# Kernel tuning notes

Hardware: AMD Instinct MI355X
Metric: run time of the kernel (lower is better)

Reference implementation:

```python
import jax, jax.numpy as jnp
import numpy as np

K = 3  # deform kernel size; stride = K//2 = 1, pad = K%2 = 1


def _conv3x3(x, w, b):
    y = jax.lax.conv_general_dilated(x, w, (1, 1), [(1, 1), (1, 1)],
                                     dimension_numbers=('NCHW', 'OIHW', 'NCHW'))
    return y + b[None, :, None, None]


def _channel_attention(x, w1, b1, w2, b2):
    # RCAN channel attention: GAP -> 1x1 conv -> ReLU -> 1x1 conv -> sigmoid -> scale
    y = jnp.mean(x, axis=(2, 3))                 # [N, C]
    y = jax.nn.relu(y @ w1.T + b1)               # [N, C//16]
    y = jax.nn.sigmoid(y @ w2.T + b2)            # [N, C]
    return x * y[:, :, None, None]


def _bilinear_gather(x, py, px):
    # x: [N,C,H,W]; py/px: [N,Ho,Wo] float sampling coords; zero padding outside.
    H, W = x.shape[2], x.shape[3]
    y0 = jnp.floor(py); x0 = jnp.floor(px)
    wy1 = py - y0; wx1 = px - x0
    wy0 = 1.0 - wy1; wx0 = 1.0 - wx1

    def corner(yi, xi):
        valid = (yi >= 0) & (yi <= H - 1) & (xi >= 0) & (xi <= W - 1)
        yc = jnp.clip(yi, 0, H - 1).astype(jnp.int32)
        xc = jnp.clip(xi, 0, W - 1).astype(jnp.int32)
        g = jax.vmap(lambda xb, yb, xb2: xb[:, yb, xb2])(x, yc, xc)  # [N,C,Ho,Wo]
        return g * valid[:, None, :, :].astype(x.dtype)

    return (corner(y0, x0) * (wy0 * wx0)[:, None]
            + corner(y0, x0 + 1.0) * (wy0 * wx1)[:, None]
            + corner(y0 + 1.0, x0) * (wy1 * wx0)[:, None]
            + corner(y0 + 1.0, x0 + 1.0) * (wy1 * wx1)[:, None])


def _deform_conv(x, offset, w, b, k=K, stride=1, pad=1):
    # torchvision deform_conv2d, offset_groups=1, no modulation mask.
    N, C, H, W = x.shape
    Ho = (H + 2 * pad - k) // stride + 1
    Wo = (W + 2 * pad - k) // stride + 1
    base_y = (jnp.arange(Ho) * stride - pad).astype(x.dtype)
    base_x = (jnp.arange(Wo) * stride - pad).astype(x.dtype)
    acc = jnp.zeros((N, w.shape[0], Ho, Wo), x.dtype)
    for i in range(k):
        for j in range(k):
            idx = i * k + j
            # torchvision layout: channel 2*idx is dy, 2*idx+1 is dx
            py = base_y[None, :, None] + i + offset[:, 2 * idx]
            px = base_x[None, None, :] + j + offset[:, 2 * idx + 1]
            sampled = _bilinear_gather(x, py, px)          # [N,C,Ho,Wo]
            acc = acc + jnp.einsum('nchw,oc->nohw', sampled, w[:, :, i, j])
    return acc + b[None, :, None, None]


def setup_inputs() -> dict:
    key = jax.random.key(0)
    ks = jax.random.split(key, 24)
    N, Cin, H, W = 8, 64, 192, 192
    Cout, sq = 64, Cin // 16
    s = 0.05
    inp = {
        'x': jax.random.normal(ks[0], (N, Cin, H, W), jnp.float32),
        'ref_x': jax.random.normal(ks[1], (N, 3, H, W), jnp.float32),
        'ref_w': jax.random.normal(ks[2], (Cin, 12, 3, 3), jnp.float32) * s,
        'ref_b': jnp.zeros((Cin,), jnp.float32),
        'off_w1': jax.random.normal(ks[3], (Cin, 2 * Cin, 3, 3), jnp.float32) * s,
        'off_b1': jnp.zeros((Cin,), jnp.float32),
        'ca1_w1': jax.random.normal(ks[4], (sq, Cin), jnp.float32) * s,
        'ca1_b1': jnp.zeros((sq,), jnp.float32),
        'ca1_w2': jax.random.normal(ks[5], (Cin, sq), jnp.float32) * s,
        'ca1_b2': jnp.zeros((Cin,), jnp.float32),
        'off_w2': jax.random.normal(ks[6], (Cin, Cin, 3, 3), jnp.float32) * s,
        'off_b2': jnp.zeros((Cin,), jnp.float32),
        'ca2_w1': jax.random.normal(ks[7], (sq, Cin), jnp.float32) * s,
        'ca2_b1': jnp.zeros((sq,), jnp.float32),
        'ca2_w2': jax.random.normal(ks[8], (Cin, sq), jnp.float32) * s,
        'ca2_b2': jnp.zeros((Cin,), jnp.float32),
        'off_w3': jax.random.normal(ks[9], (2 * K * K, Cin, 3, 3), jnp.float32) * 0.01,
        'off_b3': jnp.zeros((2 * K * K,), jnp.float32),
        'dcn_w': jax.random.normal(ks[10], (Cout, Cin, K, K), jnp.float32) * s,
        'dcn_b': jnp.zeros((Cout,), jnp.float32),
        'rgb_w': jax.random.normal(ks[11], (3, Cout, 3, 3), jnp.float32) * s,
        'rgb_b': jnp.zeros((3,), jnp.float32),
    }
    return inp


def reference(x, ref_x, ref_w, ref_b, off_w1, off_b1, ca1_w1, ca1_b1, ca1_w2, ca1_b2,
              off_w2, off_b2, ca2_w1, ca2_b1, ca2_w2, ca2_b2, off_w3, off_b3,
              dcn_w, dcn_b, rgb_w, rgb_b):
    # ref branch: 4-fold flip augmentation concat -> conv -> relu
    ref_cat = jnp.concatenate([ref_x, jnp.flip(ref_x, 2), jnp.flip(ref_x, 3),
                               jnp.flip(ref_x, (2, 3))], axis=1)
    ref_f = jax.nn.relu(_conv3x3(ref_cat, ref_w, ref_b))
    # offset branch
    t = jnp.concatenate([x, ref_f], axis=1)
    t = jax.nn.relu(_conv3x3(t, off_w1, off_b1))
    t = _channel_attention(t, ca1_w1, ca1_b1, ca1_w2, ca1_b2)
    t = jax.nn.relu(_conv3x3(t, off_w2, off_b2))
    t = _channel_attention(t, ca2_w1, ca2_b1, ca2_w2, ca2_b2)
    offset = _conv3x3(t, off_w3, off_b3)        # [N, 2*K*K, H, W]
    mask = offset
    xo = jax.nn.relu(_deform_conv(x, offset, dcn_w, dcn_b))
    rgb = _conv3x3(xo, rgb_w, rgb_b)
    return (xo, rgb, mask, offset)
```

## Files before the change

kernel.cpp:

```cpp
#include <hip/hip_runtime.h>
#include <hip/hip_bf16.h>
#include <math.h>

#define HH 192
#define WW 192
#define HW (192*192)

typedef __attribute__((ext_vector_type(8))) short bfrag;
typedef __attribute__((ext_vector_type(4))) float ffrag;

__device__ __forceinline__ float bf2f(ushort u){
    union { unsigned int i; float f; } c; c.i = ((unsigned int)u) << 16; return c.f;
}
__device__ __forceinline__ ushort f2bf(float f){
    __hip_bfloat16 h = __float2bfloat16(f);
    return *reinterpret_cast<ushort*>(&h);
}

__global__ __launch_bounds__(256)
void k_prep(const float* __restrict__ x, const float* __restrict__ rx,
            ushort* __restrict__ xbf, ushort* __restrict__ rcbf){
    const int n = blockIdx.y;
    const int tid = threadIdx.x;
    if (blockIdx.z == 0){
        __shared__ ushort sT[256*64];
        const int px0 = blockIdx.x * 256;
        for (int c = 0; c < 64; ++c){
            float v = x[((size_t)(n*64 + c))*HW + px0 + tid];
            int slot = (((c >> 3) ^ (tid & 7)) << 3) + (c & 7);
            sT[tid*64 + slot] = f2bf(v);
        }
        __syncthreads();
        for (int r = 0; r < 8; ++r){
            int u = r*256 + tid;
            int pl = u >> 3, g = u & 7;
            uint4 v = *(const uint4*)&sT[pl*64 + ((g ^ (pl & 7)) << 3)];
            *(uint4*)(xbf + ((size_t)n*HW + px0 + pl)*64 + g*8) = v;
        }
    } else {
        const int px = blockIdx.x*256 + tid;
        const int y = px / WW, xx = px - y*WW;
        ushort v[32];
#pragma unroll
        for (int m = 0; m < 4; ++m){
            int ry = (m & 1) ? (HH-1-y) : y;
            int rxp = (m & 2) ? (WW-1-xx) : xx;
#pragma unroll
            for (int c = 0; c < 3; ++c)
                v[m*3+c] = f2bf(rx[((size_t)(n*3+c))*HW + ry*WW + rxp]);
        }
#pragma unroll
        for (int j = 12; j < 32; ++j) v[j] = 0;
#pragma unroll
        for (int k = 0; k < 4; ++k)
            *(uint4*)(rcbf + ((size_t)n*HW + px)*32 + k*8) = *(uint4*)&v[k*8];
    }
}

__global__ void k_wfrag_all(const float* __restrict__ w0, const float* __restrict__ w1,
                            const float* __restrict__ w2, const float* __restrict__ w3,
                            const float* __restrict__ w4, const float* __restrict__ w5,
                            ushort* __restrict__ f0, ushort* __restrict__ f1,
                            ushort* __restrict__ f2, ushort* __restrict__ f3,
                            ushort* __restrict__ f4, ushort* __restrict__ f5){
    const float* w; ushort* wf; int cin_real, ncb, cout_real, mt;
    switch (blockIdx.y){
        case 0: w=w0; wf=f0; cin_real=12;  ncb=1; cout_real=64; mt=4; break;
        case 1: w=w1; wf=f1; cin_real=128; ncb=4; cout_real=64; mt=4; break;
        case 2: w=w2; wf=f2; cin_real=64;  ncb=2; cout_real=64; mt=4; break;
        case 3: w=w3; wf=f3; cin_real=64;  ncb=2; cout_real=18; mt=2; break;
        case 4: w=w4; wf=f4; cin_real=64;  ncb=2; cout_real=64; mt=4; break;
        default:w=w5; wf=f5; cin_real=64;  ncb=2; cout_real=3;  mt=1; break;
    }
    int idx = blockIdx.x*256 + threadIdx.x;
    int total = ncb*9*mt*512;
    if (idx >= total) return;
    int e = idx & 7;
    int lane = (idx >> 3) & 63;
    int rest = idx >> 9;
    int mtl = rest % mt;
    int tap = (rest / mt) % 9;
    int cb  = rest / (mt*9);
    int cout = mtl*16 + (lane & 15);
    int cin  = cb*32 + ((lane >> 4) << 3) + e;
    float v = 0.f;
    if (cout < cout_real && cin < cin_real)
        v = w[((size_t)cout*cin_real + cin)*9 + tap];
    wf[idx] = f2bf(v);
}

template<int NCB, int MT, bool SCALE, bool CONCAT, bool RELU, int OM, bool GAPP>
__device__ __forceinline__
void conv_body(const ushort* __restrict__ in0, const ushort* __restrict__ in1,
               const ushort* __restrict__ wf, const float* __restrict__ bias,
               const float* __restrict__ scale,
               ushort* __restrict__ obf, float* __restrict__ of0, float* __restrict__ of1,
               float* __restrict__ part, int cout_real)
{
    __shared__ ushort sXt[18*18*32];
    __shared__ float sG[4][4][16];
    __shared__ ushort sOut[(OM & 1) ? 8*16*64 : 1];
    const int tid = threadIdx.x;
    const int lane = tid & 63;
    const int wv = tid >> 6;
    const int n = blockIdx.z;
    const int ty0 = blockIdx.y*16, tx0 = blockIdx.x*16;
    const int lx = lane & 15;
    const int lg = lane >> 4;

    ffrag acc[MT][4];
#pragma unroll
    for (int mt = 0; mt < MT; ++mt)
#pragma unroll
        for (int q = 0; q < 4; ++q) acc[mt][q] = (ffrag){0.f,0.f,0.f,0.f};

    for (int cb = 0; cb < NCB; ++cb){
        __syncthreads();
        for (int u = tid; u < 1296; u += 256){
            int yy = u / 72; int rr = u - yy*72; int xx = rr >> 2; int g = rr & 3;
            int gy = ty0 - 1 + yy, gx = tx0 - 1 + xx;
            uint4 val = make_uint4(0,0,0,0);
            if (gy >= 0 && gy < HH && gx >= 0 && gx < WW){
                const ushort* src; int ch; int stride;
                if constexpr (CONCAT){
                    src = (cb < 2) ? in0 : in1;
                    ch = (cb & 1)*32 + g*8;
                    stride = 64;
                } else {
                    src = in0; ch = cb*32 + g*8; stride = NCB*32;
                }
                val = *(const uint4*)(src + ((size_t)n*HW + gy*WW + gx)*stride + ch);
                if constexpr (SCALE){
                    ushort* e = (ushort*)&val;
                    int cb8 = cb*32 + g*8;
#pragma unroll
                    for (int j = 0; j < 8; ++j)
                        e[j] = f2bf(bf2f(e[j]) * scale[n*64 + cb8 + j]);
                }
            }
            *(uint4*)&sXt[((yy*18 + xx)*4 + (g ^ ((xx >> 1) & 3)))*8] = val;
        }
        __syncthreads();

        const bfrag* wbase = (const bfrag*)wf + (size_t)cb*9*MT*64 + lane;
        bfrag a[MT];
#pragma unroll
        for (int mt = 0; mt < MT; ++mt) a[mt] = wbase[mt*64];

#pragma unroll
        for (int tap = 0; tap < 9; ++tap){
            const int ky = tap / 3, kx = tap % 3;
            bfrag an[MT];
            if (tap < 8){
#pragma unroll
                for (int mt = 0; mt < MT; ++mt) an[mt] = wbase[(tap+1)*MT*64 + mt*64];
            }
#pragma unroll
            for (int q = 0; q < 4; ++q){
                const int yl = wv*4 + q + ky;
                const int xl = lx + kx;
                bfrag b = *(const bfrag*)&sXt[((yl*18 + xl)*4 + (lg ^ ((xl >> 1) & 3)))*8];
#pragma unroll
                for (int mt = 0; mt < MT; ++mt)
                    acc[mt][q] = __builtin_amdgcn_mfma_f32_16x16x32_bf16(a[mt], b, acc[mt][q], 0, 0, 0);
            }
            if (tap < 8){
#pragma unroll
                for (int mt = 0; mt < MT; ++mt) a[mt] = an[mt];
            }
        }
    }
    const int gx = tx0 + lx;
    float psum[MT][4];
    if constexpr (GAPP){
#pragma unroll
        for (int mt = 0; mt < MT; ++mt)
#pragma unroll
            for (int j = 0; j < 4; ++j) psum[mt][j] = 0.f;
    }

    if constexpr (OM & 1){
#pragma unroll
        for (int pass = 0; pass < 2; ++pass){
            if ((wv >> 1) == pass){
#pragma unroll
                for (int mt = 0; mt < MT; ++mt){
                    const int co0 = mt*16 + lg*4;
                    const int t = mt*2 + (lg >> 1);
                    const int h = lg & 1;
#pragma unroll
                    for (int q = 0; q < 4; ++q){
                        const int py_loc = (wv*4 + q) & 7;
                        float r[4];
                        ushort pk[4];
#pragma unroll
                        for (int j = 0; j < 4; ++j){
                            float bv = (co0 + j < cout_real) ? bias[co0 + j] : 0.f;
                            float v = acc[mt][q][j] + bv;
                            if (RELU) v = fmaxf(v, 0.f);
                            r[j] = v;
                            pk[j] = f2bf(v);
                        }
                        if constexpr (GAPP){
#pragma unroll
                            for (int j = 0; j < 4; ++j) psum[mt][j] += r[j];
                        }
                        *(uint2*)&sOut[(py_loc*16 + lx)*64 + ((t ^ (lx & 7)) << 3) + h*4] = *(uint2*)pk;
                    }
                }
            }
            __syncthreads();
#pragma unroll
            for (int it = 0; it < 4; ++it){
                int u = it*256 + tid;
                int p = u >> 3, t = u & 7;
                int py = p >> 4, px = p & 15;
                uint4 v = *(const uint4*)&sOut[(py*16 + px)*64 + ((t ^ (px & 7)) << 3)];
                *(uint4*)(obf + ((size_t)n*HW + (size_t)(ty0 + pass*8 + py)*WW + tx0 + px)*64 + t*8) = v;
            }
            __syncthreads();
        }
    } else {
#pragma unroll
        for (int mt = 0; mt < MT; ++mt){
            const int co0 = mt*16 + lg*4;
#pragma unroll
            for (int q = 0; q < 4; ++q){
                const int gy = ty0 + wv*4 + q;
                float r[4];
#pragma unroll
                for (int j = 0; j < 4; ++j){
                    float bv = (co0 + j < cout_real) ? bias[co0 + j] : 0.f;
                    float v = acc[mt][q][j] + bv;
                    if (RELU) v = fmaxf(v, 0.f);
                    r[j] = v;
                }
                if constexpr (GAPP){
#pragma unroll
                    for (int j = 0; j < 4; ++j) psum[mt][j] += r[j];
                }
#pragma unroll
                for (int j = 0; j < 4; ++j){
                    int c = co0 + j;
                    if (c < cout_real){
                        size_t o = ((size_t)(n*cout_real + c))*HW + (size_t)gy*WW + gx;
                        of0[o] = r[j];
                        if (of1) of1[o] = r[j];
                    }
                }
            }
        }
    }

    if constexpr (GAPP){
#pragma unroll
        for (int mt = 0; mt < MT; ++mt)
#pragma unroll
            for (int j = 0; j < 4; ++j){
                float v = psum[mt][j];
#pragma unroll
                for (int d = 1; d < 16; d <<= 1) v += __shfl_xor(v, d, 64);
                if (lx == 0) sG[wv][lg][mt*4 + j] = v;
            }
        __syncthreads();
        if (tid < 64){
            int mt = tid >> 4, lgc = (tid >> 2) & 3, j = tid & 3;
            float s = sG[0][lgc][mt*4+j] + sG[1][lgc][mt*4+j]
                    + sG[2][lgc][mt*4+j] + sG[3][lgc][mt*4+j];
            part[(((size_t)n*144) + blockIdx.y*12 + blockIdx.x)*64 + tid] = s;
        }
    }
}

__global__ __launch_bounds__(256, 2)
void kc_ref(const ushort* __restrict__ in0, const ushort* __restrict__ wf,
            const float* __restrict__ bias, ushort* __restrict__ obf){
    conv_body<1,4,false,false,true,1,false>(in0, nullptr, wf, bias, nullptr, obf, nullptr, nullptr, nullptr, 64);
}
__global__ __launch_bounds__(256, 2)
void kc_off1(const ushort* __restrict__ in0, const ushort* __restrict__ in1,
             const ushort* __restrict__ wf, const float* __restrict__ bias,
             ushort* __restrict__ obf, float* __restrict__ part){
    conv_body<4,4,false,true,true,1,true>(in0, in1, wf, bias, nullptr, obf, nullptr, nullptr, part, 64);
}
__global__ __launch_bounds__(256, 2)
void kc_off2(const ushort* __restrict__ in0, const ushort* __restrict__ wf,
             const float* __restrict__ bias, const float* __restrict__ scale,
             ushort* __restrict__ obf, float* __restrict__ part){
    conv_body<2,4,true,false,true,1,true>(in0, nullptr, wf, bias, scale, obf, nullptr, nullptr, part, 64);
}
__global__ __launch_bounds__(256, 2)
void kc_off3(const ushort* __restrict__ in0, const ushort* __restrict__ wf,
             const float* __restrict__ bias, const float* __restrict__ scale,
             float* __restrict__ of0, float* __restrict__ of1){
    conv_body<2,2,true,false,false,2,false>(in0, nullptr, wf, bias, scale, nullptr, of0, of1, nullptr, 18);
}
__global__ __launch_bounds__(256, 2)
void kc_rgb(const ushort* __restrict__ in0, const ushort* __restrict__ wf,
            const float* __restrict__ bias, float* __restrict__ of0){
    conv_body<2,1,false,false,false,2,false>(in0, nullptr, wf, bias, nullptr, nullptr, of0, nullptr, nullptr, 3);
}

__global__ void k_cafc(const float* __restrict__ part, const float* __restrict__ w1,
                       const float* __restrict__ b1, const float* __restrict__ w2,
                       const float* __restrict__ b2, float* __restrict__ s)
{
    int n = blockIdx.x;
    int c = threadIdx.x;
    __shared__ float y[64], z[4];
    float acc = 0.f;
    for (int b = 0; b < 144; ++b) acc += part[((size_t)n*144 + b)*64 + c];
    y[c] = acc * (1.f/(float)HW);
    __syncthreads();
    if (c < 4){
        float a = b1[c];
        for (int i = 0; i < 64; ++i) a = fmaf(w1[c*64+i], y[i], a);
        z[c] = fmaxf(a, 0.f);
    }
    __syncthreads();
    float a = b2[c];
#pragma unroll
    for (int q = 0; q < 4; ++q) a = fmaf(w2[c*4+q], z[q], a);
    s[n*64+c] = 1.f/(1.f+expf(-a));
}

__global__ __launch_bounds__(256, 2)
void k_dcnm(const ushort* __restrict__ xbf, const float* __restrict__ off,
            const ushort* __restrict__ wf, const float* __restrict__ bias,
            float* __restrict__ xo, ushort* __restrict__ xobf)
{
    __shared__ ushort sS[2][128*64];
    const int tid = threadIdx.x;
    const int lane = tid & 63;
    const int wv = tid >> 6;
    const int n = blockIdx.z;
    const int ty0 = blockIdx.y*8, tx0 = blockIdx.x*16;
    const int lx = lane & 15;
    const int lg = lane >> 4;
    const int gx_out = tx0 + lx;
    const int gp = tid >> 2;
    const int gg = tid & 3;

    const ushort* xn = xbf + (size_t)n*HW*64;
    const float* offn = off + (size_t)n*18*HW;

    ffrag acc[4][2];
#pragma unroll
    for (int mt = 0; mt < 4; ++mt)
#pragma unroll
        for (int q = 0; q < 2; ++q) acc[mt][q] = (ffrag){0.f,0.f,0.f,0.f};

    int buf = 0;
    for (int tap = 0; tap < 9; ++tap){
        const int ti = tap/3, tj = tap%3;
#pragma unroll
        for (int pass = 0; pass < 2; ++pass){
            const int p = pass*64 + gp;
            const int py_ = ty0 + (p >> 4), px_ = tx0 + (p & 15);
            float dy = offn[(size_t)(2*tap)*HW + py_*WW + px_];
            float dx = offn[(size_t)(2*tap+1)*HW + py_*WW + px_];
            float sy = (float)(py_ + ti - 1) + dy;
            float sx = (float)(px_ + tj - 1) + dx;
            float y0f = floorf(sy), x0f = floorf(sx);
            float wy1 = sy - y0f, wx1 = sx - x0f;
            float wy0 = 1.f - wy1, wx0 = 1.f - wx1;
            int y0 = (int)y0f, x0 = (int)x0f;
            int y1 = y0+1, x1 = x0+1;
            float vy0 = (y0 >= 0 && y0 < HH) ? 1.f : 0.f;
            float vy1 = (y1 >= 0 && y1 < HH) ? 1.f : 0.f;
            float vx0 = (x0 >= 0 && x0 < WW) ? 1.f : 0.f;
            float vx1 = (x1 >= 0 && x1 < WW) ? 1.f : 0.f;
            float w00 = wy0*wx0*vy0*vx0, w01 = wy0*wx1*vy0*vx1;
            float w10 = wy1*wx0*vy1*vx0, w11 = wy1*wx1*vy1*vx1;
            int yc0 = min(max(y0,0),HH-1), yc1 = min(max(y1,0),HH-1);
            int xc0 = min(max(x0,0),WW-1), xc1 = min(max(x1,0),WW-1);
            int b00 = (yc0*WW + xc0)*64, b01 = (yc0*WW + xc1)*64;
            int b10 = (yc1*WW + xc0)*64, b11 = (yc1*WW + xc1)*64;
#pragma unroll
            for (int cb = 0; cb < 2; ++cb){
                const int ch = cb*32 + gg*8;
                uint4 c00 = *(const uint4*)(xn + b00 + ch);
                uint4 c01 = *(const uint4*)(xn + b01 + ch);
                uint4 c10 = *(const uint4*)(xn + b10 + ch);
                uint4 c11 = *(const uint4*)(xn + b11 + ch);
                const ushort* e00 = (const ushort*)&c00;
                const ushort* e01 = (const ushort*)&c01;
                const ushort* e10 = (const ushort*)&c10;
                const ushort* e11 = (const ushort*)&c11;
                ushort pk[8];
#pragma unroll
                for (int j = 0; j < 8; ++j){
                    float s = bf2f(e00[j])*w00 + bf2f(e01[j])*w01
                            + bf2f(e10[j])*w10 + bf2f(e11[j])*w11;
                    pk[j] = f2bf(s);
                }
                const int sl = (cb*4 + gg) ^ (p & 7);
                *(uint4*)&sS[buf][p*64 + sl*8] = *(uint4*)pk;
            }
        }
        __syncthreads();
#pragma unroll
        for (int cb = 0; cb < 2; ++cb){
            const bfrag* wbase = (const bfrag*)wf + ((size_t)(cb*9 + tap)*4)*64 + lane;
            bfrag a[4];
#pragma unroll
            for (int mt = 0; mt < 4; ++mt) a[mt] = wbase[mt*64];
#pragma unroll
            for (int q = 0; q < 2; ++q){
                const int p = (wv*2 + q)*16 + lx;
                const int sl = (cb*4 + lg) ^ (p & 7);
                bfrag b = *(const bfrag*)&sS[buf][p*64 + sl*8];
#pragma unroll
                for (int mt = 0; mt < 4; ++mt)
                    acc[mt][q] = __builtin_amdgcn_mfma_f32_16x16x32_bf16(a[mt], b, acc[mt][q], 0, 0, 0);
            }
        }
        buf ^= 1;
    }
    __syncthreads();
#pragma unroll
    for (int mt = 0; mt < 4; ++mt){
        const int co0 = mt*16 + lg*4;
        const int t = mt*2 + (lg >> 1);
        const int h = lg & 1;
#pragma unroll
        for (int q = 0; q < 2; ++q){
            const int gy = ty0 + wv*2 + q;
            const int p = (wv*2 + q)*16 + lx;
            float r[4];
            ushort pk[4];
#pragma unroll
            for (int j = 0; j < 4; ++j){
                r[j] = fmaxf(acc[mt][q][j] + bias[co0+j], 0.f);
                pk[j] = f2bf(r[j]);
            }
#pragma unroll
            for (int j = 0; j < 4; ++j)
                xo[((size_t)(n*64 + co0 + j))*HW + (size_t)gy*WW + gx_out] = r[j];
            *(uint2*)&sS[0][p*64 + ((t ^ (lx & 7)) << 3) + h*4] = *(uint2*)pk;
        }
    }
    __syncthreads();
#pragma unroll
    for (int it = 0; it < 4; ++it){
        int u = it*256 + tid;
        int p = u >> 3, t = u & 7;
        int py = p >> 4, px = p & 15;
        uint4 v = *(const uint4*)&sS[0][p*64 + ((t ^ (px & 7)) << 3)];
        *(uint4*)(xobf + ((size_t)n*HW + (size_t)(ty0 + py)*WW + tx0 + px)*64 + t*8) = v;
    }
}

extern "C" void kernel_launch(void* const* d_in, const int* in_sizes, int n_in,
                              void* d_out, int out_size, void* d_ws, size_t ws_size,
                              hipStream_t stream)
{
    const float* x      = (const float*)d_in[0];
    const float* ref_x  = (const float*)d_in[1];
    const float* ref_w  = (const float*)d_in[2];
    const float* ref_b  = (const float*)d_in[3];
    const float* off_w1 = (const float*)d_in[4];
    const float* off_b1 = (const float*)d_in[5];
    const float* ca1_w1 = (const float*)d_in[6];
    const float* ca1_b1 = (const float*)d_in[7];
    const float* ca1_w2 = (const float*)d_in[8];
    const float* ca1_b2 = (const float*)d_in[9];
    const float* off_w2 = (const float*)d_in[10];
    const float* off_b2 = (const float*)d_in[11];
    const float* ca2_w1 = (const float*)d_in[12];
    const float* ca2_b1 = (const float*)d_in[13];
    const float* ca2_w2 = (const float*)d_in[14];
    const float* ca2_b2 = (const float*)d_in[15];
    const float* off_w3 = (const float*)d_in[16];
    const float* off_b3 = (const float*)d_in[17];
    const float* dcn_w  = (const float*)d_in[18];
    const float* dcn_b  = (const float*)d_in[19];
    const float* rgb_w  = (const float*)d_in[20];
    const float* rgb_b  = (const float*)d_in[21];

    float* out = (float*)d_out;
    const size_t XO  = (size_t)8 * 64 * HW;
    const size_t RGB = (size_t)8 * 3 * HW;
    const size_t OFF = (size_t)8 * 18 * HW;
    float* xo_out   = out;
    float* rgb_out  = out + XO;
    float* mask_out = out + XO + RGB;
    float* off_out  = out + XO + RGB + OFF;

    const size_t NPX = (size_t)8 * HW;
    ushort* ws16  = (ushort*)d_ws;
    ushort* x_bf  = ws16;
    ushort* bufP  = x_bf + NPX*64;
    ushort* bufQ  = bufP + NPX*64;
    ushort* rc_bf = bufQ + NPX*64;
    ushort* wf_ref = rc_bf + NPX*32;
    ushort* wf_1   = wf_ref + 18432;
    ushort* wf_2   = wf_1 + 73728;
    ushort* wf_3   = wf_2 + 36864;
    ushort* wf_d   = wf_3 + 18432;
    ushort* wf_r   = wf_d + 36864;
    float*  part1  = (float*)(wf_r + 9216);
    float*  part2  = part1 + 73728;
    float*  s1     = part2 + 73728;
    float*  s2     = s1 + 512;

    dim3 pg(144, 8, 2), cg(12, 12, 8), dg(12, 24, 8);

    k_prep<<<pg, 256, 0, stream>>>(x, ref_x, x_bf, rc_bf);
    k_wfrag_all<<<dim3(288, 6), 256, 0, stream>>>(
        ref_w, off_w1, off_w2, off_w3, dcn_w, rgb_w,
        wf_ref, wf_1, wf_2, wf_3, wf_d, wf_r);

    kc_ref<<<cg, 256, 0, stream>>>(rc_bf, wf_ref, ref_b, bufP);
    kc_off1<<<cg, 256, 0, stream>>>(x_bf, bufP, wf_1, off_b1, bufQ, part1);
    k_cafc<<<8, 64, 0, stream>>>(part1, ca1_w1, ca1_b1, ca1_w2, ca1_b2, s1);
    kc_off2<<<cg, 256, 0, stream>>>(bufQ, wf_2, off_b2, s1, bufP, part2);
    k_cafc<<<8, 64, 0, stream>>>(part2, ca2_w1, ca2_b1, ca2_w2, ca2_b2, s2);
    kc_off3<<<cg, 256, 0, stream>>>(bufP, wf_3, off_b3, s2, off_out, mask_out);
    k_dcnm<<<dg, 256, 0, stream>>>(x_bf, off_out, wf_d, dcn_b, xo_out, bufQ);
    kc_rgb<<<cg, 256, 0, stream>>>(bufQ, wf_r, rgb_b, rgb_out);
}
```

Before: 317.4 us.

## Register-prefetch next channel block's input halo tile during MFMA compute

Adds a PF template path to the conv body that holds the next channel block's 18x18 input halo in registers, six uint4 values per thread. These loads are issued right after the shared-memory stage, so they overlap with the MFMA work on the current block and are written to LDS at the start of the next iteration. The goal is to hide global-load latency that the old load-then-compute loop left exposed. The cost is 24 extra VGPRs per thread, which under launch_bounds(256,2) could raise register pressure or cause spills, and it is enabled for all multi-block convs and the 2-block ones.

```diff
diff --git a/kernel.cpp b/kernel.cpp
--- a/kernel.cpp
+++ b/kernel.cpp
@@ -89,7 +89,7 @@
     wf[idx] = f2bf(v);
 }
 
-template<int NCB, int MT, bool SCALE, bool CONCAT, bool RELU, int OM, bool GAPP>
+template<int NCB, int MT, bool SCALE, bool CONCAT, bool RELU, int OM, bool GAPP, bool PF>
 __device__ __forceinline__
 void conv_body(const ushort* __restrict__ in0, const ushort* __restrict__ in1,
                const ushort* __restrict__ wf, const float* __restrict__ bias,
@@ -108,39 +108,76 @@
     const int lx = lane & 15;
     const int lg = lane >> 4;
 
+    uint4 rIn[PF ? 6 : 1];
+
+    auto ld_elem = [&](int cb, int u) -> uint4 {
+        int yy = u / 72; int rr = u - yy*72; int xx = rr >> 2; int g = rr & 3;
+        int gy = ty0 - 1 + yy, gx = tx0 - 1 + xx;
+        uint4 val = make_uint4(0,0,0,0);
+        if (gy >= 0 && gy < HH && gx >= 0 && gx < WW){
+            const ushort* src; int ch; int stride;
+            if constexpr (CONCAT){
+                src = (cb < 2) ? in0 : in1;
+                ch = (cb & 1)*32 + g*8;
+                stride = 64;
+            } else {
+                src = in0; ch = cb*32 + g*8; stride = NCB*32;
+            }
+            val = *(const uint4*)(src + ((size_t)n*HW + gy*WW + gx)*stride + ch);
+        }
+        return val;
+    };
+    auto st_elem = [&](int cb, int u, uint4 val){
+        int yy = u / 72; int rr = u - yy*72; int xx = rr >> 2; int g = rr & 3;
+        if constexpr (SCALE){
+            int gy = ty0 - 1 + yy, gx = tx0 - 1 + xx;
+            if (gy >= 0 && gy < HH && gx >= 0 && gx < WW){
+                ushort* e = (ushort*)&val;
+                int cb8 = cb*32 + g*8;
+#pragma unroll
+                for (int j = 0; j < 8; ++j)
+                    e[j] = f2bf(bf2f(e[j]) * scale[n*64 + cb8 + j]);
+            }
+        }
+        *(uint4*)&sXt[((yy*18 + xx)*4 + (g ^ ((xx >> 1) & 3)))*8] = val;
+    };
+
     ffrag acc[MT][4];
 #pragma unroll
     for (int mt = 0; mt < MT; ++mt)
 #pragma unroll
         for (int q = 0; q < 4; ++q) acc[mt][q] = (ffrag){0.f,0.f,0.f,0.f};
+
+    if constexpr (PF){
+#pragma unroll
+        for (int k = 0; k < 6; ++k){
+            int u = tid + k*256;
+            rIn[k] = (u < 1296) ? ld_elem(0, u) : make_uint4(0,0,0,0);
+        }
+    }
 
     for (int cb = 0; cb < NCB; ++cb){
         __syncthreads();
-        for (int u = tid; u < 1296; u += 256){
-            int yy = u / 72; int rr = u - yy*72; int xx = rr >> 2; int g = rr & 3;
-            int gy = ty0 - 1 + yy, gx = tx0 - 1 + xx;
-            uint4 val = make_uint4(0,0,0,0);
-            if (gy >= 0 && gy < HH && gx >= 0 && gx < WW){
-                const ushort* src; int ch; int stride;
-                if constexpr (CONCAT){
-                    src = (cb < 2) ? in0 : in1;
-                    ch = (cb & 1)*32 + g*8;
-                    stride = 64;
-                } else {
-                    src = in0; ch = cb*32 + g*8; stride = NCB*32;
+        if constexpr (PF){
+#pragma unroll
+            for (int k = 0; k < 6; ++k){
+                int u = tid + k*256;
+                if (u < 1296) st_elem(cb, u, rIn[k]);
+            }
+        } else {
+            for (int u = tid; u < 1296; u += 256)
+                st_elem(cb, u, ld_elem(cb, u));
+        }
+        __syncthreads();
+        if constexpr (PF){
+            if (cb + 1 < NCB){
+#pragma unroll
+                for (int k = 0; k < 6; ++k){
+                    int u = tid + k*256;
+                    rIn[k] = (u < 1296) ? ld_elem(cb + 1, u) : make_uint4(0,0,0,0);
                 }
-                val = *(const uint4*)(src + ((size_t)n*HW + gy*WW + gx)*stride + ch);
-                if constexpr (SCALE){
-                    ushort* e = (ushort*)&val;
-                    int cb8 = cb*32 + g*8;
-#pragma unroll
-                    for (int j = 0; j < 8; ++j)
-                        e[j] = f2bf(bf2f(e[j]) * scale[n*64 + cb8 + j]);
-                }
-            }
-            *(uint4*)&sXt[((yy*18 + xx)*4 + (g ^ ((xx >> 1) & 3)))*8] = val;
-        }
-        __syncthreads();
+            }
+        }
 
         const bfrag* wbase = (const bfrag*)wf + (size_t)cb*9*MT*64 + lane;
         bfrag a[MT];
@@ -275,30 +312,30 @@
 __global__ __launch_bounds__(256, 2)
 void kc_ref(const ushort* __restrict__ in0, const ushort* __restrict__ wf,
             const float* __restrict__ bias, ushort* __restrict__ obf){
-    conv_body<1,4,false,false,true,1,false>(in0, nullptr, wf, bias, nullptr, obf, nullptr, nullptr, nullptr, 64);
+    conv_body<1,4,false,false,true,1,false,false>(in0, nullptr, wf, bias, nullptr, obf, nullptr, nullptr, nullptr, 64);
 }
 __global__ __launch_bounds__(256, 2)
 void kc_off1(const ushort* __restrict__ in0, const ushort* __restrict__ in1,
              const ushort* __restrict__ wf, const float* __restrict__ bias,
              ushort* __restrict__ obf, float* __restrict__ part){
-    conv_body<4,4,false,true,true,1,true>(in0, in1, wf, bias, nullptr, obf, nullptr, nullptr, part, 64);
+    conv_body<4,4,false,true,true,1,true,true>(in0, in1, wf, bias, nullptr, obf, nullptr, nullptr, part, 64);
 }
 __global__ __launch_bounds__(256, 2)
 void kc_off2(const ushort* __restrict__ in0, const ushort* __restrict__ wf,
              const float* __restrict__ bias, const float* __restrict__ scale,
              ushort* __restrict__ obf, float* __restrict__ part){
-    conv_body<2,4,true,false,true,1,true>(in0, nullptr, wf, bias, scale, obf, nullptr, nullptr, part, 64);
+    conv_body<2,4,true,false,true,1,true,true>(in0, nullptr, wf, bias, scale, obf, nullptr, nullptr, part, 64);
 }
 __global__ __launch_bounds__(256, 2)
 void kc_off3(const ushort* __restrict__ in0, const ushort* __restrict__ wf,
              const float* __restrict__ bias, const float* __restrict__ scale,
              float* __restrict__ of0, float* __restrict__ of1){
-    conv_body<2,2,true,false,false,2,false>(in0, nullptr, wf, bias, scale, nullptr, of0, of1, nullptr, 18);
+    conv_body<2,2,true,false,false,2,false,true>(in0, nullptr, wf, bias, scale, nullptr, of0, of1, nullptr, 18);
 }
 __global__ __launch_bounds__(256, 2)
 void kc_rgb(const ushort* __restrict__ in0, const ushort* __restrict__ wf,
             const float* __restrict__ bias, float* __restrict__ of0){
-    conv_body<2,1,false,false,false,2,false>(in0, nullptr, wf, bias, nullptr, nullptr, of0, nullptr, nullptr, 3);
+    conv_body<2,1,false,false,false,2,false,true>(in0, nullptr, wf, bias, nullptr, nullptr, of0, nullptr, nullptr, 3);
 }
 
 __global__ void k_cafc(const float* __restrict__ part, const float* __restrict__ w1,
```

After: 337.0 us. 6.2% more time.
